# Optimization experiments

Measured on AMD Instinct MI355X. Metric: run time of the kernel, lower is better.

## Reference

```python
import jax, jax.numpy as jnp
import numpy as np

THR1 = 0.8     # lif1 threshold
THR2 = 1.0     # lif2 (Synaptic) default threshold
ALPHA2 = 0.9   # Synaptic alpha (not learnable, use_stdp=False)
BETA2 = 0.8    # Synaptic beta
SLOPE = 25.0   # snntorch fast_sigmoid default slope

@jax.custom_vjp
def fast_sigmoid_spike(x):
    return (x > 0).astype(x.dtype)

def _fs_fwd(x):
    return fast_sigmoid_spike(x), x

def _fs_bwd(x, g):
    return (g / (SLOPE * jnp.abs(x) + 1.0) ** 2,)

fast_sigmoid_spike.defvjp(_fs_fwd, _fs_bwd)

@jax.custom_vjp
def atan_spike(x):  # snntorch default ATan surrogate, alpha=2.0
    return (x > 0).astype(x.dtype)

def _at_fwd(x):
    return atan_spike(x), x

def _at_bwd(x, g):
    return (g / (1.0 + (jnp.pi * x) ** 2),)

atan_spike.defvjp(_at_fwd, _at_bwd)

def setup_inputs() -> dict:
    key = jax.random.key(0)
    k = jax.random.split(key, 6)
    B, S, V, H, E, T = 16, 16, 16000, 512, 256, 20
    x = jax.random.randint(k[0], (B, S), 0, V)
    embed_w = jax.random.normal(k[1], (V, E), dtype=jnp.float32)  # torch Embedding ~ N(0,1)
    fc1_w = jax.random.normal(k[2], (H, E), dtype=jnp.float32) / np.sqrt(E)
    fc1_b = jax.random.normal(k[3], (H,), dtype=jnp.float32) / np.sqrt(E)
    fc2_w = jax.random.normal(k[4], (V, H), dtype=jnp.float32) / np.sqrt(H)
    fc2_b = jax.random.normal(k[5], (V,), dtype=jnp.float32) / np.sqrt(H)
    beta1 = jnp.float32(0.85)  # learnable Leaky beta
    return {"x": x, "embed_w": embed_w, "fc1_w": fc1_w, "fc1_b": fc1_b,
            "fc2_w": fc2_w, "fc2_b": fc2_b, "beta1": beta1, "time_steps": T}

def reference(x, embed_w, fc1_w, fc1_b, fc2_w, fc2_b, beta1, time_steps):
    B, S = x.shape
    H = fc1_w.shape[0]
    V = fc2_w.shape[0]
    emb = embed_w[x]                       # [B, S, 256]
    b1 = jnp.clip(beta1, 0.0, 1.0)
    mem1 = jnp.zeros((B, H), emb.dtype)
    syn2 = jnp.zeros((B, V), emb.dtype)
    mem2 = jnp.zeros((B, V), emb.dtype)

    def token_step(carry, emb_t):          # emb_t: [B, 256]
        mem1, syn2, mem2 = carry
        cur1 = emb_t @ fc1_w.T + fc1_b     # identical every inner step (hoisted)

        def inner(c, _):
            m1, s2, m2, _ = c
            reset = fast_sigmoid_spike(m1 - THR1)          # reset from previous mem
            m1 = b1 * m1 + cur1 - reset * THR1             # Leaky, subtract reset
            spk1 = fast_sigmoid_spike(m1 - THR1)
            cur2 = spk1 @ fc2_w.T + fc2_b                  # [B, V]
            s2 = ALPHA2 * s2 + cur2                        # Synaptic, reset='none'
            m2 = BETA2 * m2 + s2
            spk2 = atan_spike(m2 - THR2)
            return (m1, s2, m2, spk2), None

        (mem1, syn2, mem2, spk2), _ = jax.lax.scan(
            inner, (mem1, syn2, mem2, jnp.zeros_like(mem2)), None, length=time_steps)
        return (mem1, syn2, mem2), spk2    # keep last spk2 of inner loop

    (mem1, syn2, mem2), outs = jax.lax.scan(
        token_step, (mem1, syn2, mem2), jnp.swapaxes(emb, 0, 1))  # scan over seq
    out = jnp.transpose(outs, (1, 0, 2))   # [B, S, V]
    return out, mem1, syn2, mem2
```

## Files before the change

### kernel.cpp

```cpp
#include <hip/hip_runtime.h>

#define Bdim 16
#define Sdim 16
#define Edim 256
#define Hdim 512
#define Vdim 16000
#define THR1f 0.8f
#define THR2f 1.0f

typedef unsigned int   u32;
typedef unsigned short u16;
typedef __attribute__((ext_vector_type(8))) short bf16x8;
typedef __attribute__((ext_vector_type(4))) float f32x4;
typedef __attribute__((ext_vector_type(4))) u32   u32x4;

__device__ __forceinline__ u16 f2bf(float f) {
  u32 u = __float_as_uint(f);
  return (u16)((u + 0x7FFFu + ((u >> 16) & 1u)) >> 16);
}
__device__ __forceinline__ u32 pack2(float a, float b) {
  return (u32)f2bf(a) | ((u32)f2bf(b) << 16);
}

__global__ __launch_bounds__(256) void snn_prep(
    const int* __restrict__ x, const float* __restrict__ embed_w,
    const float* __restrict__ fc1_w, const float* __restrict__ fc1_b,
    const float* __restrict__ beta1p, const int* __restrict__ tsp,
    u16* __restrict__ Ab3, float* __restrict__ mem1)
{
  __shared__ __align__(16) float As[64][68];
  __shared__ __align__(16) float Ws[64][68];
  __shared__ float cbuf[64][68];
  __shared__ int sidx[64];
  const int tid = threadIdx.x;
  const int n0  = blockIdx.x * 64;
  const int bi0 = blockIdx.y * 4;
  const int tx = tid & 15, ty = tid >> 4;

  if (tid < 64) sidx[tid] = x[(bi0 + (tid & 3)) * Sdim + (tid >> 2)];

  float acc[4][4] = {{0.f}};
  for (int k0 = 0; k0 < Edim; k0 += 64) {
    __syncthreads();
#pragma unroll
    for (int i = 0; i < 16; ++i) {
      const int k = tid + i * 256;
      const int rr = k >> 6, j = k & 63;
      As[j][rr] = embed_w[(size_t)sidx[rr] * Edim + k0 + j];
      Ws[j][rr] = fc1_w[(size_t)(n0 + rr) * Edim + k0 + j];
    }
    __syncthreads();
#pragma unroll
    for (int j = 0; j < 64; ++j) {
      const float4 av = *(const float4*)&As[j][ty * 4];
      const float4 wv = *(const float4*)&Ws[j][tx * 4];
      const float a[4] = {av.x, av.y, av.z, av.w};
      const float w[4] = {wv.x, wv.y, wv.z, wv.w};
#pragma unroll
      for (int i = 0; i < 4; ++i)
#pragma unroll
        for (int jj = 0; jj < 4; ++jj)
          acc[i][jj] = fmaf(a[i], w[jj], acc[i][jj]);
    }
  }
#pragma unroll
  for (int i = 0; i < 4; ++i)
#pragma unroll
    for (int jj = 0; jj < 4; ++jj)
      cbuf[ty * 4 + i][tx * 4 + jj] = acc[i][jj] + fc1_b[n0 + tx * 4 + jj];
  __syncthreads();

  const int bb = tid >> 6, hl = tid & 63;
  const int b  = bi0 + bb;
  const int hg = n0 + hl;
  const float b1 = fminf(fmaxf(beta1p[0], 0.f), 1.f);
  const int T = tsp[0];

  double w9T = 1.0, w8T = 1.0;
  for (int i = 0; i < T; ++i) { w9T *= 0.9; w8T *= 0.8; }

  const int S = hg >> 5, q = (hg >> 3) & 3, jc = hg & 7;

  float m1 = 0.f;
  for (int t = 0; t < Sdim; ++t) {
    const float cur = cbuf[t * 4 + bb][hl];
    double p9 = w9T, p8 = w8T;
    float cs = 0.f, cm = 0.f;
    for (int u = 0; u < T; ++u) {
      const float reset = (m1 > THR1f) ? THR1f : 0.f;
      m1 = b1 * m1 + cur - reset;
      if (m1 > THR1f) {
        cs += (float)(p9 * (10.0 / 9.0));
        cm += (float)(10.0 * (p9 - p8));
      }
      p9 *= (10.0 / 9.0);
      p8 *= 1.25;
    }
    int rb = 2 * b;
    int R  = 2 * t + (rb >> 4);
    int l  = q * 16 + (rb & 15);
    Ab3[((size_t)(S * 32 + R) * 64 + l) * 8 + jc] = f2bf(cs);
    rb = 2 * b + 1;
    R  = 2 * t + (rb >> 4);
    l  = q * 16 + (rb & 15);
    Ab3[((size_t)(S * 32 + R) * 64 + l) * 8 + jc] = f2bf(cm);
  }
  mem1[b * Hdim + hg] = m1;
}

__global__ __launch_bounds__(512, 2) void snn_fused(
    const u16* __restrict__ Ab3, const float* __restrict__ W,
    const float* __restrict__ fc2_b, const int* __restrict__ tsp,
    float* __restrict__ out, float* __restrict__ syn2, float* __restrict__ mem2)
{
  __shared__ float2 st[16][64];
  const int tid  = threadIdx.x;
  const int lane = tid & 63;
  const int wr   = tid >> 6;
  const int v0   = blockIdx.x * 64;
  const int col  = lane & 15;
  const int grp  = lane >> 4;

  f32x4 acc[4][4];
#pragma unroll
  for (int i = 0; i < 4; ++i)
#pragma unroll
    for (int c = 0; c < 4; ++c)
#pragma unroll
      for (int e = 0; e < 4; ++e) acc[i][c][e] = 0.f;

  const char* abase = (const char*)Ab3 + (wr << 12) + lane * 16;
  const float* wp0 = W + (size_t)(v0 + 0  + col) * Hdim + grp * 8;
  const float* wp1 = W + (size_t)(v0 + 16 + col) * Hdim + grp * 8;
  const float* wp2 = W + (size_t)(v0 + 32 + col) * Hdim + grp * 8;
  const float* wp3 = W + (size_t)(v0 + 48 + col) * Hdim + grp * 8;

  bf16x8 aBuf[2][4];
  float4 wBuf[2][8];

#pragma unroll
  for (int i = 0; i < 4; ++i)
    aBuf[0][i] = *(const bf16x8*)(abase + i * 1024);
  wBuf[0][0] = *(const float4*)(wp0);     wBuf[0][1] = *(const float4*)(wp0 + 4);
  wBuf[0][2] = *(const float4*)(wp1);     wBuf[0][3] = *(const float4*)(wp1 + 4);
  wBuf[0][4] = *(const float4*)(wp2);     wBuf[0][5] = *(const float4*)(wp2 + 4);
  wBuf[0][6] = *(const float4*)(wp3);     wBuf[0][7] = *(const float4*)(wp3 + 4);

#pragma unroll
  for (int S = 0; S < 16; ++S) {
    const int cur = S & 1, nxt = cur ^ 1;
    if (S < 15) {
      const int o = (S + 1) * 32;
#pragma unroll
      for (int i = 0; i < 4; ++i)
        aBuf[nxt][i] = *(const bf16x8*)(abase + (S + 1) * 32768 + i * 1024);
      wBuf[nxt][0] = *(const float4*)(wp0 + o);
      wBuf[nxt][1] = *(const float4*)(wp0 + o + 4);
      wBuf[nxt][2] = *(const float4*)(wp1 + o);
      wBuf[nxt][3] = *(const float4*)(wp1 + o + 4);
      wBuf[nxt][4] = *(const float4*)(wp2 + o);
      wBuf[nxt][5] = *(const float4*)(wp2 + o + 4);
      wBuf[nxt][6] = *(const float4*)(wp3 + o);
      wBuf[nxt][7] = *(const float4*)(wp3 + o + 4);
    }
    bf16x8 bfr[4];
#pragma unroll
    for (int c = 0; c < 4; ++c) {
      const float4 a = wBuf[cur][2 * c], b = wBuf[cur][2 * c + 1];
      u32x4 bw;
      bw.x = pack2(a.x, a.y); bw.y = pack2(a.z, a.w);
      bw.z = pack2(b.x, b.y); bw.w = pack2(b.z, b.w);
      bfr[c] = __builtin_bit_cast(bf16x8, bw);
    }
#pragma unroll
    for (int i = 0; i < 4; ++i)
#pragma unroll
      for (int c = 0; c < 4; ++c)
        acc[i][c] = __builtin_amdgcn_mfma_f32_16x16x32_bf16(
            aBuf[cur][i], bfr[c], acc[i][c], 0, 0, 0);
  }

  const int T = tsp[0];
  double p9 = 1.0, p8 = 1.0;
  for (int i = 0; i < T; ++i) { p9 *= 0.9; p8 *= 0.8; }
  const float Ps  = (float)p9;
  const float Pm  = (float)p8;
  const float Pms = (float)(0.9 * 10.0 * (p9 - p8));
  const float Sws = (float)(10.0 * (1.0 - p9));
  const float Swm = (float)(10.0 * (9.0 * (1.0 - p9) - 4.0 * (1.0 - p8)));

  float bbs[4], bbm[4];
#pragma unroll
  for (int c = 0; c < 4; ++c) {
    const float bb = fc2_b[v0 + c * 16 + col];
    bbs[c] = bb * Sws;
    bbm[c] = bb * Swm;
  }

  for (int s = 0; s < 8; ++s) {
    if (wr == s) {
      float s2[4][4], m2[4][4];
#pragma unroll
      for (int c = 0; c < 4; ++c)
#pragma unroll
        for (int hi = 0; hi < 2; ++hi)
#pragma unroll
          for (int j = 0; j < 2; ++j) {
            const int b = 8 * hi + 2 * grp + j;
            if (s > 0) {
              const float2 v2 = st[b][c * 16 + col];
              s2[c][hi * 2 + j] = v2.x; m2[c][hi * 2 + j] = v2.y;
            } else {
              s2[c][hi * 2 + j] = 0.f; m2[c][hi * 2 + j] = 0.f;
            }
          }
#pragma unroll
      for (int tt = 0; tt < 2; ++tt) {
        const int t = 2 * s + tt;
#pragma unroll
        for (int c = 0; c < 4; ++c)
#pragma unroll
          for (int hi = 0; hi < 2; ++hi)
#pragma unroll
            for (int j = 0; j < 2; ++j) {
              const int b  = 8 * hi + 2 * grp + j;
              const int si = hi * 2 + j;
              const float gs = acc[2 * tt + hi][c][2 * j];
              const float gm = acc[2 * tt + hi][c][2 * j + 1];
              const float m2n = Pm * m2[c][si] + Pms * s2[c][si] + gm + bbm[c];
              s2[c][si] = Ps * s2[c][si] + gs + bbs[c];
              m2[c][si] = m2n;
              out[((size_t)b * Sdim + t) * Vdim + v0 + c * 16 + col] =
                  (m2n > THR2f) ? 1.f : 0.f;
            }
      }
#pragma unroll
      for (int c = 0; c < 4; ++c)
#pragma unroll
        for (int hi = 0; hi < 2; ++hi)
#pragma unroll
          for (int j = 0; j < 2; ++j) {
            const int b  = 8 * hi + 2 * grp + j;
            const int si = hi * 2 + j;
            if (s < 7) {
              st[b][c * 16 + col] = make_float2(s2[c][si], m2[c][si]);
            } else {
              syn2[(size_t)b * Vdim + v0 + c * 16 + col] = s2[c][si];
              mem2[(size_t)b * Vdim + v0 + c * 16 + col] = m2[c][si];
            }
          }
    }
    __syncthreads();
  }
}

extern "C" void kernel_launch(void* const* d_in, const int* in_sizes, int n_in,
                              void* d_out, int out_size, void* d_ws, size_t ws_size,
                              hipStream_t stream) {
  const int*   x       = (const int*)d_in[0];
  const float* embed_w = (const float*)d_in[1];
  const float* fc1_w   = (const float*)d_in[2];
  const float* fc1_b   = (const float*)d_in[3];
  const float* fc2_w   = (const float*)d_in[4];
  const float* fc2_b   = (const float*)d_in[5];
  const float* beta1   = (const float*)d_in[6];
  const int*   tsteps  = (const int*)d_in[7];

  float* out  = (float*)d_out;
  float* mem1 = out + (size_t)Bdim * Sdim * Vdim;
  float* syn2 = mem1 + (size_t)Bdim * Hdim;
  float* mem2 = syn2 + (size_t)Bdim * Vdim;

  u16* Ab3 = (u16*)d_ws;

  snn_prep<<<dim3(8, 4), 256, 0, stream>>>(x, embed_w, fc1_w, fc1_b,
                                           beta1, tsteps, Ab3, mem1);
  snn_fused<<<Vdim / 64, 512, 0, stream>>>(Ab3, fc2_w, fc2_b, tsteps,
                                           out, syn2, mem2);
}
```

Before: 169.2 us.

## Pre-convert fc2 weights to bf16 MFMA layout and halve fused block width

Adds 4000 blocks to the prep kernel that convert fc2_w from fp32 to bf16 and write it in a swizzled layout matching the MFMA operand order. The fused kernel can then load bf16 B fragments directly instead of converting fp32 on the fly. Each fused block now covers 32 vocab columns instead of 64, which doubles the grid to 500 blocks and raises the launch-bounds occupancy hint to 4. The cost is that the full weight matrix is converted to bf16 on every call, an extra read of 32MB plus a write of 16MB to workspace, which may outweigh the halved weight traffic in the fused kernel.

```diff
diff --git a/kernel.cpp b/kernel.cpp
--- a/kernel.cpp
+++ b/kernel.cpp
@@ -12,7 +12,6 @@
 typedef unsigned short u16;
 typedef __attribute__((ext_vector_type(8))) short bf16x8;
 typedef __attribute__((ext_vector_type(4))) float f32x4;
-typedef __attribute__((ext_vector_type(4))) u32   u32x4;
 
 __device__ __forceinline__ u16 f2bf(float f) {
   u32 u = __float_as_uint(f);
@@ -22,19 +21,37 @@
   return (u32)f2bf(a) | ((u32)f2bf(b) << 16);
 }
 
-__global__ __launch_bounds__(256) void snn_prep(
+__global__ __launch_bounds__(256) void snn_pre(
     const int* __restrict__ x, const float* __restrict__ embed_w,
     const float* __restrict__ fc1_w, const float* __restrict__ fc1_b,
-    const float* __restrict__ beta1p, const int* __restrict__ tsp,
-    u16* __restrict__ Ab3, float* __restrict__ mem1)
+    const float* __restrict__ W2, const float* __restrict__ beta1p,
+    const int* __restrict__ tsp,
+    u16* __restrict__ Ab3, u16* __restrict__ Wb, float* __restrict__ mem1)
 {
+  const int tid = threadIdx.x;
+
+  if (blockIdx.x < 4000) {
+    const int gid = blockIdx.x * 256 + tid;
+    const int v   = gid >> 6;
+    const int kg  = gid & 63;
+    const float4* s = (const float4*)(W2 + (size_t)v * Hdim + kg * 8);
+    const float4 a = s[0], b = s[1];
+    uint4 o;
+    o.x = pack2(a.x, a.y); o.y = pack2(a.z, a.w);
+    o.z = pack2(b.x, b.y); o.w = pack2(b.z, b.w);
+    const size_t dst = ((size_t)((v >> 4) * 16 + (kg >> 2)) * 64 +
+                        ((v & 15) + 16 * (kg & 3))) * 16;
+    *(uint4*)((char*)Wb + dst) = o;
+    return;
+  }
+
   __shared__ __align__(16) float As[64][68];
   __shared__ __align__(16) float Ws[64][68];
   __shared__ float cbuf[64][68];
   __shared__ int sidx[64];
-  const int tid = threadIdx.x;
-  const int n0  = blockIdx.x * 64;
-  const int bi0 = blockIdx.y * 4;
+  const int pb  = blockIdx.x - 4000;
+  const int n0  = (pb & 7) * 64;
+  const int bi0 = (pb >> 3) * 4;
   const int tx = tid & 15, ty = tid >> 4;
 
   if (tid < 64) sidx[tid] = x[(bi0 + (tid & 3)) * Sdim + (tid >> 2)];
@@ -108,76 +125,64 @@
   mem1[b * Hdim + hg] = m1;
 }
 
-__global__ __launch_bounds__(512, 2) void snn_fused(
-    const u16* __restrict__ Ab3, const float* __restrict__ W,
+__global__ __launch_bounds__(512, 4) void snn_fused(
+    const u16* __restrict__ Ab3, const u16* __restrict__ Wb,
     const float* __restrict__ fc2_b, const int* __restrict__ tsp,
     float* __restrict__ out, float* __restrict__ syn2, float* __restrict__ mem2)
 {
-  __shared__ float2 st[16][64];
+  __shared__ float2 st[16][32];
   const int tid  = threadIdx.x;
   const int lane = tid & 63;
   const int wr   = tid >> 6;
-  const int v0   = blockIdx.x * 64;
+  const int v0   = blockIdx.x * 32;
   const int col  = lane & 15;
   const int grp  = lane >> 4;
 
-  f32x4 acc[4][4];
+  f32x4 acc[4][2];
 #pragma unroll
   for (int i = 0; i < 4; ++i)
 #pragma unroll
-    for (int c = 0; c < 4; ++c)
+    for (int c = 0; c < 2; ++c)
 #pragma unroll
       for (int e = 0; e < 4; ++e) acc[i][c][e] = 0.f;
 
   const char* abase = (const char*)Ab3 + (wr << 12) + lane * 16;
-  const float* wp0 = W + (size_t)(v0 + 0  + col) * Hdim + grp * 8;
-  const float* wp1 = W + (size_t)(v0 + 16 + col) * Hdim + grp * 8;
-  const float* wp2 = W + (size_t)(v0 + 32 + col) * Hdim + grp * 8;
-  const float* wp3 = W + (size_t)(v0 + 48 + col) * Hdim + grp * 8;
-
-  bf16x8 aBuf[2][4];
-  float4 wBuf[2][8];
-
-#pragma unroll
-  for (int i = 0; i < 4; ++i)
-    aBuf[0][i] = *(const bf16x8*)(abase + i * 1024);
-  wBuf[0][0] = *(const float4*)(wp0);     wBuf[0][1] = *(const float4*)(wp0 + 4);
-  wBuf[0][2] = *(const float4*)(wp1);     wBuf[0][3] = *(const float4*)(wp1 + 4);
-  wBuf[0][4] = *(const float4*)(wp2);     wBuf[0][5] = *(const float4*)(wp2 + 4);
-  wBuf[0][6] = *(const float4*)(wp3);     wBuf[0][7] = *(const float4*)(wp3 + 4);
-
-#pragma unroll
-  for (int S = 0; S < 16; ++S) {
-    const int cur = S & 1, nxt = cur ^ 1;
-    if (S < 15) {
-      const int o = (S + 1) * 32;
+  const char* bbase = (const char*)Wb + ((size_t)blockIdx.x << 15) + lane * 16;
+
+  bf16x8 a0[4], a1[4], b0[2], b1[2];
+#pragma unroll
+  for (int i = 0; i < 4; ++i) a0[i] = *(const bf16x8*)(abase + i * 1024);
+#pragma unroll
+  for (int c = 0; c < 2; ++c) b0[c] = *(const bf16x8*)(bbase + c * 16384);
+
+#pragma unroll
+  for (int Sp = 0; Sp < 16; Sp += 2) {
+#pragma unroll
+    for (int i = 0; i < 4; ++i)
+      a1[i] = *(const bf16x8*)(abase + (Sp + 1) * 32768 + i * 1024);
+#pragma unroll
+    for (int c = 0; c < 2; ++c)
+      b1[c] = *(const bf16x8*)(bbase + c * 16384 + (Sp + 1) * 1024);
+#pragma unroll
+    for (int i = 0; i < 4; ++i)
+#pragma unroll
+      for (int c = 0; c < 2; ++c)
+        acc[i][c] = __builtin_amdgcn_mfma_f32_16x16x32_bf16(
+            a0[i], b0[c], acc[i][c], 0, 0, 0);
+    if (Sp + 2 < 16) {
 #pragma unroll
       for (int i = 0; i < 4; ++i)
-        aBuf[nxt][i] = *(const bf16x8*)(abase + (S + 1) * 32768 + i * 1024);
-      wBuf[nxt][0] = *(const float4*)(wp0 + o);
-      wBuf[nxt][1] = *(const float4*)(wp0 + o + 4);
-      wBuf[nxt][2] = *(const float4*)(wp1 + o);
-      wBuf[nxt][3] = *(const float4*)(wp1 + o + 4);
-      wBuf[nxt][4] = *(const float4*)(wp2 + o);
-      wBuf[nxt][5] = *(const float4*)(wp2 + o + 4);
-      wBuf[nxt][6] = *(const float4*)(wp3 + o);
-      wBuf[nxt][7] = *(const float4*)(wp3 + o + 4);
-    }
-    bf16x8 bfr[4];
-#pragma unroll
-    for (int c = 0; c < 4; ++c) {
-      const float4 a = wBuf[cur][2 * c], b = wBuf[cur][2 * c + 1];
-      u32x4 bw;
-      bw.x = pack2(a.x, a.y); bw.y = pack2(a.z, a.w);
-      bw.z = pack2(b.x, b.y); bw.w = pack2(b.z, b.w);
-      bfr[c] = __builtin_bit_cast(bf16x8, bw);
+        a0[i] = *(const bf16x8*)(abase + (Sp + 2) * 32768 + i * 1024);
+#pragma unroll
+      for (int c = 0; c < 2; ++c)
+        b0[c] = *(const bf16x8*)(bbase + c * 16384 + (Sp + 2) * 1024);
     }
 #pragma unroll
     for (int i = 0; i < 4; ++i)
 #pragma unroll
-      for (int c = 0; c < 4; ++c)
+      for (int c = 0; c < 2; ++c)
         acc[i][c] = __builtin_amdgcn_mfma_f32_16x16x32_bf16(
-            aBuf[cur][i], bfr[c], acc[i][c], 0, 0, 0);
+            a1[i], b1[c], acc[i][c], 0, 0, 0);
   }
 
   const int T = tsp[0];
@@ -189,9 +194,9 @@
   const float Sws = (float)(10.0 * (1.0 - p9));
   const float Swm = (float)(10.0 * (9.0 * (1.0 - p9) - 4.0 * (1.0 - p8)));
 
-  float bbs[4], bbm[4];
-#pragma unroll
-  for (int c = 0; c < 4; ++c) {
+  float bbs[2], bbm[2];
+#pragma unroll
+  for (int c = 0; c < 2; ++c) {
     const float bb = fc2_b[v0 + c * 16 + col];
     bbs[c] = bb * Sws;
     bbm[c] = bb * Swm;
@@ -199,9 +204,9 @@
 
   for (int s = 0; s < 8; ++s) {
     if (wr == s) {
-      float s2[4][4], m2[4][4];
-#pragma unroll
-      for (int c = 0; c < 4; ++c)
+      float s2[2][4], m2[2][4];
+#pragma unroll
+      for (int c = 0; c < 2; ++c)
 #pragma unroll
         for (int hi = 0; hi < 2; ++hi)
 #pragma unroll
@@ -218,7 +223,7 @@
       for (int tt = 0; tt < 2; ++tt) {
         const int t = 2 * s + tt;
 #pragma unroll
-        for (int c = 0; c < 4; ++c)
+        for (int c = 0; c < 2; ++c)
 #pragma unroll
           for (int hi = 0; hi < 2; ++hi)
 #pragma unroll
@@ -235,7 +240,7 @@
             }
       }
 #pragma unroll
-      for (int c = 0; c < 4; ++c)
+      for (int c = 0; c < 2; ++c)
 #pragma unroll
         for (int hi = 0; hi < 2; ++hi)
 #pragma unroll
@@ -272,9 +277,10 @@
   float* mem2 = syn2 + (size_t)Bdim * Vdim;
 
   u16* Ab3 = (u16*)d_ws;
-
-  snn_prep<<<dim3(8, 4), 256, 0, stream>>>(x, embed_w, fc1_w, fc1_b,
-                                           beta1, tsteps, Ab3, mem1);
-  snn_fused<<<Vdim / 64, 512, 0, stream>>>(Ab3, fc2_w, fc2_b, tsteps,
+  u16* Wb  = (u16*)((char*)d_ws + 524288);
+
+  snn_pre<<<4032, 256, 0, stream>>>(x, embed_w, fc1_w, fc1_b, fc2_w,
+                                    beta1, tsteps, Ab3, Wb, mem1);
+  snn_fused<<<Vdim / 32, 512, 0, stream>>>(Ab3, Wb, fc2_b, tsteps,
                                            out, syn2, mem2);
 }
```

After: 155.0 us. 8.4% less time.
